# Performance work log

Measured on AMD Instinct MI355X. Metric: run time of the kernel, lower is better.

Reference implementation:

```python
import jax, jax.numpy as jnp
import numpy as np

B, L = 512, 200
WORD_V, PATH_V = 100000, 200000
E, D = 128, 384


def setup_inputs() -> dict:
    key = jax.random.key(0)
    ks = jax.random.split(key, 10)
    inp = {
        "x_s1": jax.random.randint(ks[0], (B, L), 0, WORD_V),
        "path1": jax.random.randint(ks[1], (B, L), 0, PATH_V),
        "x_t1": jax.random.randint(ks[2], (B, L), 0, WORD_V),
        "x_s2": jax.random.randint(ks[3], (B, L), 0, WORD_V),
        "path2": jax.random.randint(ks[4], (B, L), 0, PATH_V),
        "x_t2": jax.random.randint(ks[5], (B, L), 0, WORD_V),
        # learned parameters
        "word_emb": jax.random.normal(ks[6], (WORD_V, E), dtype=jnp.float32) * 0.02,
        "path_emb": jax.random.normal(ks[7], (PATH_V, E), dtype=jnp.float32) * 0.02,
        "W_fc": jax.random.normal(ks[8], (D, 3 * E), dtype=jnp.float32) * (1.0 / np.sqrt(3 * E)),  # nn.Linear weight [out, in], no bias
        "attn": jax.random.uniform(ks[9], (D, 1), dtype=jnp.float32),
    }
    return inp


def _extract(xs, path, xt, word_emb, path_emb, W_fc, attn):
    # gather + concat -> [B, L, 3E]
    ctx = jnp.concatenate([word_emb[xs], path_emb[path], word_emb[xt]], axis=-1)
    # linear (no bias, dropout is identity at eval) + tanh -> [B, L, D]
    h = jnp.tanh(jnp.einsum('blf,df->bld', ctx, W_fc))
    # attention scores [B, L, 1]; the zeros mask in the original is a no-op
    scores = jnp.einsum('bld,do->blo', h, attn)
    a = jax.nn.softmax(scores, axis=1)
    code_vec = jnp.sum(h * a, axis=1)  # [B, D]
    return code_vec, a


def reference(x_s1, path1, x_t1, x_s2, path2, x_t2, word_emb, path_emb, W_fc, attn):
    cv1, _ = _extract(x_s1, path1, x_t1, word_emb, path_emb, W_fc, attn)
    cv2, _ = _extract(x_s2, path2, x_t2, word_emb, path_emb, W_fc, attn)
    return (cv1, cv2)
```

## Files before the change

### kernel.cpp

```cpp
#include <hip/hip_runtime.h>
#include <hip/hip_bf16.h>

#define B_N 512
#define L_N 200
#define E_N 128
#define K_N 384
#define D_N 384

typedef __bf16 v8bf  __attribute__((ext_vector_type(8)));
typedef float  v4f   __attribute__((ext_vector_type(4)));
typedef unsigned int v4u __attribute__((ext_vector_type(4)));
typedef unsigned short v8us __attribute__((ext_vector_type(8)));

__device__ __forceinline__ unsigned short f2bf(float f) {
    union { __bf16 b; unsigned short u; } cv;
    cv.b = (__bf16)f;
    return cv.u;
}
__device__ __forceinline__ float fast_tanh(float x) {
    float e = __expf(2.f * x);
    return 1.f - 2.f * __builtin_amdgcn_rcpf(e + 1.f);
}

__global__ void pack_w(const float* __restrict__ W, unsigned short* __restrict__ Wp) {
    int gid  = blockIdx.x * 256 + threadIdx.x;
    int lane = gid & 63;
    int u    = gid >> 6;
    int gn   = u % 24;
    int kk   = u / 24;
    int c    = lane & 15, quad = lane >> 4;
    const float* src = W + (gn * 16 + c) * K_N + kk * 32 + quad * 8;
    ushort4 lo, hi;
    lo.x = f2bf(src[0]); lo.y = f2bf(src[1]); lo.z = f2bf(src[2]); lo.w = f2bf(src[3]);
    hi.x = f2bf(src[4]); hi.y = f2bf(src[5]); hi.z = f2bf(src[6]); hi.w = f2bf(src[7]);
    ushort4* dst = (ushort4*)(Wp + (size_t)gid * 8);
    dst[0] = lo; dst[1] = hi;
}

#define SEG_E 4096

template<int MT>
__device__ __forceinline__ void mfma_chunk(
    const unsigned short* Alds, const v4u* wp4,
    int wv, int lane, int quad, int c, v4f (&acc)[2][3])
{
    const int arow = c * 128;
    const int akey = (c & 7) << 3;
    const int q8   = quad * 8;

    #pragma unroll 2
    for (int kk = 0; kk < 12; ++kk) {
        v8bf b0 = __builtin_bit_cast(v8bf, wp4[(kk * 24 + wv * 3 + 0) * 64 + lane]);
        v8bf b1 = __builtin_bit_cast(v8bf, wp4[(kk * 24 + wv * 3 + 1) * 64 + lane]);
        v8bf b2 = __builtin_bit_cast(v8bf, wp4[(kk * 24 + wv * 3 + 2) * 64 + lane]);
        const int soff = (((kk & 3) * 32 + q8) ^ akey);
        #pragma unroll
        for (int mt = 0; mt < MT; ++mt) {
            v8bf a = *(const v8bf*)&Alds[(kk >> 2) * SEG_E + mt * 2048 + arow + soff];
            acc[mt][0] = __builtin_amdgcn_mfma_f32_16x16x32_bf16(a, b0, acc[mt][0], 0, 0, 0);
            acc[mt][1] = __builtin_amdgcn_mfma_f32_16x16x32_bf16(a, b1, acc[mt][1], 0, 0, 0);
            acc[mt][2] = __builtin_amdgcn_mfma_f32_16x16x32_bf16(a, b2, acc[mt][2], 0, 0, 0);
        }
    }
}

template<int MT>
__device__ __forceinline__ void tanh_score(
    float (*sp)[32], int wv, int quad, int c,
    float an0, float an1, float an2, v4f (&acc)[2][3])
{
    #pragma unroll
    for (int mt = 0; mt < MT; ++mt) {
        #pragma unroll
        for (int r = 0; r < 4; ++r) {
            float h0 = fast_tanh(acc[mt][0][r]);
            float h1 = fast_tanh(acc[mt][1][r]);
            float h2 = fast_tanh(acc[mt][2][r]);
            acc[mt][0][r] = h0; acc[mt][1][r] = h1; acc[mt][2][r] = h2;
            float sv = h0 * an0 + h1 * an1 + h2 * an2;
            sv += __shfl_xor(sv, 1);
            sv += __shfl_xor(sv, 2);
            sv += __shfl_xor(sv, 4);
            sv += __shfl_xor(sv, 8);
            if (c == 0) sp[wv][mt * 16 + quad * 4 + r] = sv;
        }
    }
}

__global__ __launch_bounds__(512, 4)
void c2v_fused(const int* __restrict__ xs1, const int* __restrict__ ph1,
               const int* __restrict__ xt1,
               const int* __restrict__ xs2, const int* __restrict__ ph2,
               const int* __restrict__ xt2,
               const float* __restrict__ wemb, const float* __restrict__ pemb,
               const unsigned short* __restrict__ Wp,
               const float* __restrict__ attn,
               float* __restrict__ out)
{
    const int tid  = threadIdx.x;
    const int wv   = tid >> 6;
    const int lane = tid & 63;
    const int quad = lane >> 4;
    const int c    = lane & 15;
    const int b    = blockIdx.x;
    const int pass = blockIdx.y;

    const int* xs = pass ? xs2 : xs1;
    const int* ph = pass ? ph2 : ph1;
    const int* xt = pass ? xt2 : xt1;

    __shared__ __align__(16) unsigned short Alds[3 * SEG_E];
    __shared__ float sp[8][32];
    __shared__ int   ilds[3 * 208];

    for (int u = tid; u < 624; u += 512) {
        int s = u / 208, g = u - s * 208;
        const int* tab = (s == 0) ? xs : (s == 1) ? ph : xt;
        ilds[u] = (g < L_N) ? tab[b * L_N + g] : 0;
    }

    const float an0 = attn[(wv * 3 + 0) * 16 + c];
    const float an1 = attn[(wv * 3 + 1) * 16 + c];
    const float an2 = attn[(wv * 3 + 2) * 16 + c];

    float o0 = 0.f, o1 = 0.f, o2 = 0.f;
    float Mrun = -1e30f, Zrun = 0.f;

    const v4u* wp4 = (const v4u*)Wp;

    const int sm = tid >> 4;
    const int sj = tid & 15;

    __syncthreads();

    for (int chunk = 0; chunk < 7; ++chunk) {
        const int row0  = chunk * 32;
        const int mrows = (chunk == 6) ? 16 : 32;
        const int mtmax = (chunk == 6) ? 1 : 2;

        const int  sg  = row0 + sm;
        const bool act = (sm < mrows) && (sg < L_N);
        float4 fa[3], fb[3];
        #pragma unroll
        for (int s = 0; s < 3; ++s) {
            if (act) {
                const float* eb = (s == 1) ? pemb : wemb;
                const float* src = eb + (size_t)ilds[s * 208 + sg] * E_N + sj * 8;
                fa[s] = *(const float4*)src;
                fb[s] = *(const float4*)(src + 4);
            } else {
                fa[s].x = fa[s].y = fa[s].z = fa[s].w = 0.f;
                fb[s] = fa[s];
            }
        }
        v8us cv[3];
        #pragma unroll
        for (int s = 0; s < 3; ++s) {
            cv[s][0] = f2bf(fa[s].x); cv[s][1] = f2bf(fa[s].y);
            cv[s][2] = f2bf(fa[s].z); cv[s][3] = f2bf(fa[s].w);
            cv[s][4] = f2bf(fb[s].x); cv[s][5] = f2bf(fb[s].y);
            cv[s][6] = f2bf(fb[s].z); cv[s][7] = f2bf(fb[s].w);
        }

        __syncthreads();

        if (sm < mrows) {
            const int soff = sm * 128 + ((sj * 8) ^ ((sm & 7) << 3));
            #pragma unroll
            for (int s = 0; s < 3; ++s)
                *(v8us*)&Alds[s * SEG_E + soff] = cv[s];
        }
        __syncthreads();

        v4f acc[2][3];
        #pragma unroll
        for (int i = 0; i < 2; ++i)
            #pragma unroll
            for (int j = 0; j < 3; ++j)
                acc[i][j] = (v4f){0.f, 0.f, 0.f, 0.f};

        if (chunk < 6) {
            mfma_chunk<2>(Alds, wp4, wv, lane, quad, c, acc);
            tanh_score<2>(sp, wv, quad, c, an0, an1, an2, acc);
        } else {
            mfma_chunk<1>(Alds, wp4, wv, lane, quad, c, acc);
            tanh_score<1>(sp, wv, quad, c, an0, an1, an2, acc);
        }
        __syncthreads();

        {
            int g = row0 + lane;
            float s = -1e30f;
            if (lane < 32) {
                float t = sp[0][lane] + sp[1][lane] + sp[2][lane] + sp[3][lane]
                        + sp[4][lane] + sp[5][lane] + sp[6][lane] + sp[7][lane];
                if (g < L_N) s = t;
            }
            float mx = s;
            #pragma unroll
            for (int off = 32; off > 0; off >>= 1) mx = fmaxf(mx, __shfl_xor(mx, off));
            float Mnew  = fmaxf(Mrun, mx);
            float alpha = __expf(Mrun - Mnew);
            float e = (lane < 32 && g < L_N) ? __expf(s - Mnew) : 0.f;
            float zc = e;
            #pragma unroll
            for (int off = 32; off > 0; off >>= 1) zc += __shfl_xor(zc, off);
            Zrun = Zrun * alpha + zc;
            Mrun = Mnew;

            float p0 = 0.f, p1 = 0.f, p2 = 0.f;
            #pragma unroll
            for (int mt = 0; mt < 2; ++mt) {
                if (mt < mtmax) {
                    #pragma unroll
                    for (int r = 0; r < 4; ++r) {
                        float w = __shfl(e, mt * 16 + quad * 4 + r);
                        p0 += w * acc[mt][0][r];
                        p1 += w * acc[mt][1][r];
                        p2 += w * acc[mt][2][r];
                    }
                }
            }
            o0 = o0 * alpha + p0;
            o1 = o1 * alpha + p1;
            o2 = o2 * alpha + p2;
        }
    }

    const float zinv = __builtin_amdgcn_rcpf(Zrun);

    float* outp = out + (size_t)(pass * B_N + b) * D_N;
    o0 += __shfl_xor(o0, 16); o0 += __shfl_xor(o0, 32);
    o1 += __shfl_xor(o1, 16); o1 += __shfl_xor(o1, 32);
    o2 += __shfl_xor(o2, 16); o2 += __shfl_xor(o2, 32);
    if (quad == 0) {
        outp[(wv * 3 + 0) * 16 + c] = o0 * zinv;
        outp[(wv * 3 + 1) * 16 + c] = o1 * zinv;
        outp[(wv * 3 + 2) * 16 + c] = o2 * zinv;
    }
}

extern "C" void kernel_launch(void* const* d_in, const int* in_sizes, int n_in,
                              void* d_out, int out_size, void* d_ws, size_t ws_size,
                              hipStream_t stream) {
    unsigned short* Wp = (unsigned short*)d_ws;
    pack_w<<<72, 256, 0, stream>>>((const float*)d_in[8], Wp);
    dim3 grid(B_N, 2, 1);
    c2v_fused<<<grid, 512, 0, stream>>>(
        (const int*)d_in[0], (const int*)d_in[1], (const int*)d_in[2],
        (const int*)d_in[3], (const int*)d_in[4], (const int*)d_in[5],
        (const float*)d_in[6], (const float*)d_in[7],
        Wp, (const float*)d_in[9],
        (float*)d_out);
}
```

Baseline: 306.6 us.

## Prefetch next chunk's embedding rows via global_load_lds during MFMA

```diff
diff --git a/kernel.cpp b/kernel.cpp
--- a/kernel.cpp
+++ b/kernel.cpp
@@ -109,12 +109,13 @@
     const int* ph = pass ? ph2 : ph1;
     const int* xt = pass ? xt2 : xt1;
 
+    __shared__ __align__(16) float f32buf[3 * 4096];
     __shared__ __align__(16) unsigned short Alds[3 * SEG_E];
     __shared__ float sp[8][32];
-    __shared__ int   ilds[3 * 208];
-
-    for (int u = tid; u < 624; u += 512) {
-        int s = u / 208, g = u - s * 208;
+    __shared__ int   ilds[3 * 224];
+
+    for (int u = tid; u < 672; u += 512) {
+        int s = u / 224, g = u - s * 224;
         const int* tab = (s == 0) ? xs : (s == 1) ? ph : xt;
         ilds[u] = (g < L_N) ? tab[b * L_N + g] : 0;
     }
@@ -127,49 +128,56 @@
     float Mrun = -1e30f, Zrun = 0.f;
 
     const v4u* wp4 = (const v4u*)Wp;
-
-    const int sm = tid >> 4;
-    const int sj = tid & 15;
-
+    const int cm = tid >> 4;
+    const int cj = tid & 15;
+
+    auto issue_gll = [&](int nc) {
+        #pragma unroll
+        for (int i = 0; i < 6; ++i) {
+            int u = (wv * 6 + i) * 64 + lane;
+            int s = u >> 10;
+            int r = u & 1023;
+            int m = r >> 5;
+            int j = r & 31;
+            int gi = ilds[s * 224 + nc * 32 + m];
+            const float* eb = (s == 1) ? pemb : wemb;
+            const float* src = eb + (size_t)gi * E_N + j * 4;
+            __builtin_amdgcn_global_load_lds(
+                (const __attribute__((address_space(1))) unsigned int*)src,
+                (__attribute__((address_space(3))) unsigned int*)&f32buf[(wv * 6 + i) * 256],
+                16, 0, 0);
+        }
+    };
+
+    auto convert_store = [&](int nc) {
+        const int  mr  = (nc == 6) ? 16 : 32;
+        const bool act = (cm < mr) && (nc * 32 + cm < L_N);
+        #pragma unroll
+        for (int s = 0; s < 3; ++s) {
+            v4f x0 = *(const v4f*)&f32buf[s * 4096 + cm * 128 + cj * 8];
+            v4f x1 = *(const v4f*)&f32buf[s * 4096 + cm * 128 + cj * 8 + 4];
+            v8us t;
+            if (act) {
+                t[0] = f2bf(x0[0]); t[1] = f2bf(x0[1]);
+                t[2] = f2bf(x0[2]); t[3] = f2bf(x0[3]);
+                t[4] = f2bf(x1[0]); t[5] = f2bf(x1[1]);
+                t[6] = f2bf(x1[2]); t[7] = f2bf(x1[3]);
+            } else {
+                t[0]=t[1]=t[2]=t[3]=t[4]=t[5]=t[6]=t[7]=0;
+            }
+            *(v8us*)&Alds[s * SEG_E + cm * 128 + ((cj * 8) ^ ((cm & 7) << 3))] = t;
+        }
+    };
+
+    __syncthreads();
+    issue_gll(0);
     __syncthreads();
 
     for (int chunk = 0; chunk < 7; ++chunk) {
         const int row0  = chunk * 32;
-        const int mrows = (chunk == 6) ? 16 : 32;
         const int mtmax = (chunk == 6) ? 1 : 2;
 
-        const int  sg  = row0 + sm;
-        const bool act = (sm < mrows) && (sg < L_N);
-        float4 fa[3], fb[3];
-        #pragma unroll
-        for (int s = 0; s < 3; ++s) {
-            if (act) {
-                const float* eb = (s == 1) ? pemb : wemb;
-                const float* src = eb + (size_t)ilds[s * 208 + sg] * E_N + sj * 8;
-                fa[s] = *(const float4*)src;
-                fb[s] = *(const float4*)(src + 4);
-            } else {
-                fa[s].x = fa[s].y = fa[s].z = fa[s].w = 0.f;
-                fb[s] = fa[s];
-            }
-        }
-        v8us cv[3];
-        #pragma unroll
-        for (int s = 0; s < 3; ++s) {
-            cv[s][0] = f2bf(fa[s].x); cv[s][1] = f2bf(fa[s].y);
-            cv[s][2] = f2bf(fa[s].z); cv[s][3] = f2bf(fa[s].w);
-            cv[s][4] = f2bf(fb[s].x); cv[s][5] = f2bf(fb[s].y);
-            cv[s][6] = f2bf(fb[s].z); cv[s][7] = f2bf(fb[s].w);
-        }
-
-        __syncthreads();
-
-        if (sm < mrows) {
-            const int soff = sm * 128 + ((sj * 8) ^ ((sm & 7) << 3));
-            #pragma unroll
-            for (int s = 0; s < 3; ++s)
-                *(v8us*)&Alds[s * SEG_E + soff] = cv[s];
-        }
+        convert_store(chunk);
         __syncthreads();
 
         v4f acc[2][3];
@@ -181,6 +189,7 @@
 
         if (chunk < 6) {
             mfma_chunk<2>(Alds, wp4, wv, lane, quad, c, acc);
+            issue_gll(chunk + 1);
             tanh_score<2>(sp, wv, quad, c, an0, an1, an2, acc);
         } else {
             mfma_chunk<1>(Alds, wp4, wv, lane, quad, c, acc);
```

New measurement: 290.0 us. 5.4% less time.
